# Kernel tuning notes

Measured on AMD Instinct MI355X. Metric: run time of the kernel, lower is better.

Reference implementation:

```python
import jax, jax.numpy as jnp
import numpy as np

DIM = 1024
NUM_HEADS = 16
HEAD_DIM = 64
SCALE = 1.0 / np.sqrt(float(HEAD_DIM))


def setup_inputs() -> dict:
    key = jax.random.key(0)
    ks = jax.random.split(key, 11)
    B, S, D = 2, 4096, DIM
    glorot = lambda k, shape: jax.random.uniform(
        k, shape, jnp.float32,
        -jnp.sqrt(6.0 / (shape[0] + shape[1])), jnp.sqrt(6.0 / (shape[0] + shape[1])))
    return {
        "x": jax.random.normal(ks[0], (B, S, D), jnp.float32),
        "Wq": glorot(ks[1], (D, NUM_HEADS * HEAD_DIM)),
        "bq": jnp.zeros((NUM_HEADS * HEAD_DIM,), jnp.float32),
        "Wk": glorot(ks[2], (D, NUM_HEADS * HEAD_DIM)),
        "bk": jnp.zeros((NUM_HEADS * HEAD_DIM,), jnp.float32),
        "Wv": glorot(ks[3], (D, NUM_HEADS * HEAD_DIM)),
        "bv": jnp.zeros((NUM_HEADS * HEAD_DIM,), jnp.float32),
        "Wqt": glorot(ks[4], (D, D)),
        "bqt": jnp.zeros((D,), jnp.float32),
        "Wo": glorot(ks[5], (D, D)),
        "bo": jnp.zeros((D,), jnp.float32),
        "num_anchor_tokens": 512,
    }


def _split_heads(t):
    # [B, T, H*Dh] -> [B, H, T, Dh]
    B, T, _ = t.shape
    return t.reshape(B, T, NUM_HEADS, HEAD_DIM).transpose(0, 2, 1, 3)


def reference(x, Wq, bq, Wk, bk, Wv, bv, Wqt, bqt, Wo, bo, num_anchor_tokens):
    B, S, D = x.shape
    A = num_anchor_tokens  # static Python int
    anchors = x[:, :A, :]            # [B, A, D]
    queries = x[:, A:, :]            # [B, S-A, D]

    anchor_q = _split_heads(anchors @ Wq + bq)   # [B, H, A, Dh]
    anchor_k = _split_heads(anchors @ Wk + bk)   # [B, H, A, Dh]
    anchor_v = _split_heads(anchors @ Wv + bv)   # [B, H, A, Dh]
    query_q = _split_heads(queries @ Wqt + bqt)  # [B, H, S-A, Dh]

    combined_q = jnp.concatenate([anchor_q, query_q], axis=2)  # [B, H, S, Dh]
    scores = jnp.einsum("bhsd,bhad->bhsa", combined_q, anchor_k) * SCALE
    attn = jax.nn.softmax(scores, axis=-1)        # [B, H, S, A]
    out = jnp.einsum("bhsa,bhad->bhsd", attn, anchor_v)  # [B, H, S, Dh]
    out = out.transpose(0, 2, 1, 3).reshape(B, S, D)
    return out @ Wo + bo
```

## Files before the change

kernel.cpp:

```cpp
#include <hip/hip_runtime.h>
#include <hip/hip_bf16.h>
#include <math.h>
#include <stdint.h>

typedef _Float16 f16;
typedef _Float16 f16x8 __attribute__((ext_vector_type(8)));
typedef _Float16 f16x4 __attribute__((ext_vector_type(4)));
typedef float f32x4 __attribute__((ext_vector_type(4)));

#define DIM   1024
#define NH    16
#define HD    64
#define BB    2
#define SS    4096
#define AA    512
#define SCALE 0.125f
#define EXP_C1 0.18033688011112043f
#define EXP_C2 (-2.8853900817779268f)

#define GLOAD_LDS16(g, l)                                                                   \
  __builtin_amdgcn_global_load_lds((const __attribute__((address_space(1))) uint32_t*)(g),  \
                                   (__attribute__((address_space(3))) uint32_t*)(l), 16, 0, 0)

static const size_t OFF_XH  = 0;
static const size_t OFF_WT  = 8388608;
static const size_t OFF_QC  = OFF_WT + 5u*1048576u;
static const size_t OFF_KB  = OFF_QC + 8388608u;
static const size_t OFF_VT  = OFF_KB + 1048576u;
static const size_t OFF_AO  = OFF_VT + 1048576u;

__global__ __launch_bounds__(256) void cast_x_kernel(const float* __restrict__ x,
                                                     f16* __restrict__ xh) {
    size_t i = ((size_t)blockIdx.x * 256 + threadIdx.x) * 4;
    float4 v = *reinterpret_cast<const float4*>(x + i);
    f16x4 o;
    o[0] = (f16)v.x; o[1] = (f16)v.y; o[2] = (f16)v.z; o[3] = (f16)v.w;
    *reinterpret_cast<f16x4*>(xh + i) = o;
}

__global__ __launch_bounds__(256) void wcast_kernel(const float* W0, const float* W1,
                                                    const float* W2, const float* W3,
                                                    const float* W4,
                                                    f16* T0, f16* T1, f16* T2, f16* T3, f16* T4) {
    __shared__ float tile[32][33];
    const float* W; f16* T;
    switch (blockIdx.z) {
        case 0: W = W0; T = T0; break;
        case 1: W = W1; T = T1; break;
        case 2: W = W2; T = T2; break;
        case 3: W = W3; T = T3; break;
        default: W = W4; T = T4; break;
    }
    int tx = threadIdx.x, ty = threadIdx.y;
    int gx = blockIdx.x * 32, gy = blockIdx.y * 32;
#pragma unroll
    for (int i = 0; i < 32; i += 8)
        tile[ty + i][tx] = W[(size_t)(gy + ty + i) * DIM + gx + tx];
    __syncthreads();
#pragma unroll
    for (int i = 0; i < 32; i += 8)
        T[(size_t)(gx + ty + i) * DIM + gy + tx] = (f16)tile[tx][ty + i];
}

#define G_STAGE(buf, k0)                                               \
    {                                                                  \
        GLOAD_LDS16(Ap + (k0), &As[buf][wid << 9]);                    \
        GLOAD_LDS16(Ap + (k0) + (size_t)64 * DIM,                      \
                    &As[buf][(wid << 9) + 2048]);                      \
        GLOAD_LDS16(Bp + (k0), &Bs[buf][wid << 9]);                    \
        GLOAD_LDS16(Bp + (k0) + (size_t)64 * DIM,                      \
                    &Bs[buf][(wid << 9) + 2048]);                      \
    }

#define G_KLOOP                                                                                   \
    G_STAGE(0, 0);                                                                                \
    __syncthreads();                                                                              \
    int cur = 0;                                                                                  \
    for (int k0 = 0; k0 < DIM; k0 += 32) {                                                        \
        if (k0 + 32 < DIM) G_STAGE(cur ^ 1, k0 + 32);                                             \
        f16x8 af[4], bf[4];                                                                       \
        _Pragma("unroll")                                                                         \
        for (int m = 0; m < 4; m++) {                                                             \
            const int r = wr + m * 16 + lr;                                                       \
            af[m] = *reinterpret_cast<const f16x8*>(&As[cur][r * 32 + ((lg ^ ((r >> 1) & 3)) << 3)]); \
        }                                                                                         \
        _Pragma("unroll")                                                                         \
        for (int n = 0; n < 4; n++) {                                                             \
            const int r = wc + n * 16 + lr;                                                       \
            bf[n] = *reinterpret_cast<const f16x8*>(&Bs[cur][r * 32 + ((lg ^ ((r >> 1) & 3)) << 3)]); \
        }                                                                                         \
        _Pragma("unroll")                                                                         \
        for (int m = 0; m < 4; m++)                                                               \
            _Pragma("unroll")                                                                     \
            for (int n = 0; n < 4; n++)                                                           \
                acc[m][n] = __builtin_amdgcn_mfma_f32_16x16x32_f16(af[m], bf[n], acc[m][n], 0, 0, 0); \
        __syncthreads();                                                                          \
        cur ^= 1;                                                                                 \
    }

__global__ __launch_bounds__(256) void proj_kernel(const f16* __restrict__ xh,
                                                   const f16* __restrict__ wtq,
                                                   const f16* __restrict__ wtqt,
                                                   const f16* __restrict__ wtk,
                                                   const f16* __restrict__ wtv,
                                                   const float* __restrict__ bq,
                                                   const float* __restrict__ bqt,
                                                   const float* __restrict__ bk,
                                                   const float* __restrict__ bv,
                                                   f16* __restrict__ qc,
                                                   f16* __restrict__ kbuf,
                                                   f16* __restrict__ vtb) {
    __shared__ __align__(16) f16 As[2][4096];
    __shared__ __align__(16) f16 Bs[2][4096];

    const int t    = threadIdx.x;
    const int wid  = t >> 6;
    const int lane = t & 63;
    const int lr   = lane & 15;
    const int lg   = lane >> 4;
    const int x    = blockIdx.x, bc = blockIdx.y;

    int b, srow0, mode, sdim;
    const f16* Bt; const float* bias; f16* outp;
    if (x < 64) {
        b = x >> 5; srow0 = (x & 31) * 128;
        if (srow0 < 512) { Bt = wtq; bias = bq; } else { Bt = wtqt; bias = bqt; }
        mode = 0; sdim = SS; outp = qc;
    } else if (x < 72) {
        int y = x - 64; b = y >> 2; srow0 = (y & 3) * 128;
        Bt = wtk; bias = bk; mode = 0; sdim = AA; outp = kbuf;
    } else {
        int y = x - 72; b = y >> 2; srow0 = (y & 3) * 128;
        Bt = wtv; bias = bv; mode = 1; sdim = AA; outp = vtb;
    }

    const int srow = (wid << 4) + (lane >> 2);
    const int sch  = ((lane & 3) ^ ((lane >> 3) & 3)) << 3;
    const f16* Ap = xh + ((size_t)b * SS + srow0 + srow) * DIM + sch;
    const f16* Bp = Bt + ((size_t)(bc * 128 + srow)) * DIM + sch;

    const int wr = (wid >> 1) * 64;
    const int wc = (wid & 1) * 64;

    f32x4 acc[4][4] = {};
    G_KLOOP

#pragma unroll
    for (int m = 0; m < 4; m++) {
        const int row_local = wr + m * 16 + lg * 4;
#pragma unroll
        for (int n = 0; n < 4; n++) {
            const int c  = bc * 128 + wc + n * 16 + lr;
            const float bvv = bias[c];
            const int h = c >> 6, d = c & 63;
#pragma unroll
            for (int q = 0; q < 4; q++) {
                const int s_g = srow0 + row_local + q;
                const float val = acc[m][n][q] + bvv;
                if (mode == 0)
                    outp[(((size_t)(b * NH + h)) * sdim + s_g) * HD + d] = (f16)val;
                else
                    outp[(((size_t)(b * NH + h)) * HD + d) * AA + s_g] = (f16)val;
            }
        }
    }
}

__global__ __launch_bounds__(256) void final_gemm(const f16* __restrict__ ao,
                                                  const f16* __restrict__ wto,
                                                  const float* __restrict__ bo,
                                                  float* __restrict__ out) {
    __shared__ __align__(16) f16 As[2][4096];
    __shared__ __align__(16) f16 Bs[2][4096];

    const int t    = threadIdx.x;
    const int wid  = t >> 6;
    const int lane = t & 63;
    const int lr   = lane & 15;
    const int lg   = lane >> 4;
    const int br   = blockIdx.x, bc = blockIdx.y;

    const int b     = br >> 5;
    const int srow0 = (br & 31) * 128;

    const int srow = (wid << 4) + (lane >> 2);
    const int sch  = ((lane & 3) ^ ((lane >> 3) & 3)) << 3;
    const f16* Ap = ao + ((size_t)b * SS + srow0 + srow) * DIM + sch;
    const f16* Bp = wto + ((size_t)(bc * 128 + srow)) * DIM + sch;

    const int wr = (wid >> 1) * 64;
    const int wc = (wid & 1) * 64;

    f32x4 acc[4][4] = {};
    G_KLOOP

#pragma unroll
    for (int m = 0; m < 4; m++) {
        const int row_local = wr + m * 16 + lg * 4;
#pragma unroll
        for (int n = 0; n < 4; n++) {
            const int c  = bc * 128 + wc + n * 16 + lr;
            const float bvv = bo[c];
#pragma unroll
            for (int q = 0; q < 4; q++)
                out[((size_t)b * SS + srow0 + row_local + q) * DIM + c] = acc[m][n][q] + bvv;
        }
    }
}

__global__ __launch_bounds__(256) void attn_kernel(const f16* __restrict__ qc,
                                                   const f16* __restrict__ kb,
                                                   const f16* __restrict__ vt,
                                                   f16* __restrict__ ao) {
    __shared__ __align__(16) f16 Ks[2][64 * 64];
    __shared__ __align__(16) f16 Vs[2][64 * 64];
    __shared__ __align__(16) f16 Ps[4][16][64];

    const int t    = threadIdx.x;
    const int wid  = t >> 6;
    const int lane = t & 63;
    const int lr   = lane & 15;
    const int lg   = lane >> 4;
    const int qt   = blockIdx.x;
    const int h    = blockIdx.y;
    const int b    = blockIdx.z;
    const size_t bh = (size_t)b * NH + h;

    f16x8 qa[2][2];
#pragma unroll
    for (int g = 0; g < 2; g++) {
        const int qrow = qt * 128 + wid * 32 + g * 16 + lr;
        const f16* qp = qc + (bh * SS + qrow) * HD + lg * 8;
        qa[g][0] = *reinterpret_cast<const f16x8*>(qp);
        qa[g][1] = *reinterpret_cast<const f16x8*>(qp + 32);
    }

    const int sr_k = wid * 16 + (lane >> 3);
    const f16* kg = kb + bh * (size_t)AA * HD;
    const f16* vg = vt + bh * (size_t)HD * AA;

    f32x4 acc[2][4] = {};
    float rsum[2][4] = {};

#define ATTN_STAGE(buf, a0)                                                          \
    {                                                                                \
        _Pragma("unroll")                                                            \
        for (int i = 0; i < 2; i++) {                                                \
            const int r  = sr_k + i * 8;                                             \
            const int ck = (((lane & 7) ^ (r & 7)) << 3);                            \
            GLOAD_LDS16(kg + (size_t)((a0) + r) * HD + ck,                           \
                        &Ks[buf][(wid * 16 + i * 8) * 64]);                          \
            GLOAD_LDS16(vg + (size_t)r * AA + (a0) + ck,                             \
                        &Vs[buf][(wid * 16 + i * 8) * 64]);                          \
        }                                                                            \
    }

    ATTN_STAGE(0, 0);
    __syncthreads();

    int cur = 0;
    for (int at = 0; at < AA / 64; ++at) {
        if (at < AA / 64 - 1) ATTN_STAGE(cur ^ 1, (at + 1) * 64);

        f32x4 s[2][4];
#pragma unroll
        for (int n = 0; n < 4; n++) {
            const int r = n * 16 + lr;
            const int xk = r & 7;
            f16x8 kf0 = *reinterpret_cast<const f16x8*>(&Ks[cur][r * 64 + ((lg ^ xk) << 3)]);
            f16x8 kf1 = *reinterpret_cast<const f16x8*>(&Ks[cur][r * 64 + (((lg + 4) ^ xk) << 3)]);
#pragma unroll
            for (int g = 0; g < 2; g++) {
                f32x4 z = {};
                z = __builtin_amdgcn_mfma_f32_16x16x32_f16(qa[g][0], kf0, z, 0, 0, 0);
                z = __builtin_amdgcn_mfma_f32_16x16x32_f16(qa[g][1], kf1, z, 0, 0, 0);
                s[g][n] = z;
            }
        }

#pragma unroll
        for (int g = 0; g < 2; g++) {
#pragma unroll
            for (int n = 0; n < 4; n++) {
#pragma unroll
                for (int q = 0; q < 4; q++) {
                    const float p = exp2f(fmaf(s[g][n][q], EXP_C1, EXP_C2));
                    rsum[g][q] += p;
                    const int row = lg * 4 + q;
                    Ps[wid][row][(((2 * n + (lr >> 3)) ^ (row & 7)) << 3) + (lr & 7)] = (f16)p;
                }
            }
            const f16x8 pa0 = *reinterpret_cast<const f16x8*>(&Ps[wid][lr][(lg ^ (lr & 7)) << 3]);
            const f16x8 pa1 = *reinterpret_cast<const f16x8*>(&Ps[wid][lr][((lg + 4) ^ (lr & 7)) << 3]);
#pragma unroll
            for (int n = 0; n < 4; n++) {
                const int d = n * 16 + lr;
                const int xv = d & 7;
                f16x8 vf0 = *reinterpret_cast<const f16x8*>(&Vs[cur][d * 64 + ((lg ^ xv) << 3)]);
                f16x8 vf1 = *reinterpret_cast<const f16x8*>(&Vs[cur][d * 64 + (((lg + 4) ^ xv) << 3)]);
                acc[g][n] = __builtin_amdgcn_mfma_f32_16x16x32_f16(pa0, vf0, acc[g][n], 0, 0, 0);
                acc[g][n] = __builtin_amdgcn_mfma_f32_16x16x32_f16(pa1, vf1, acc[g][n], 0, 0, 0);
            }
        }

        __syncthreads();
        cur ^= 1;
    }

#pragma unroll
    for (int off = 1; off < 16; off <<= 1)
#pragma unroll
        for (int g = 0; g < 2; g++)
#pragma unroll
            for (int q = 0; q < 4; q++) rsum[g][q] += __shfl_xor(rsum[g][q], off);

#pragma unroll
    for (int g = 0; g < 2; g++)
#pragma unroll
        for (int q = 0; q < 4; q++) {
            const float inv = 1.0f / rsum[g][q];
            const int row = qt * 128 + wid * 32 + g * 16 + lg * 4 + q;
#pragma unroll
            for (int n = 0; n < 4; n++)
                ao[((size_t)b * SS + row) * DIM + h * HD + n * 16 + lr] = (f16)(acc[g][n][q] * inv);
        }
}

extern "C" void kernel_launch(void* const* d_in, const int* in_sizes, int n_in,
                              void* d_out, int out_size, void* d_ws, size_t ws_size,
                              hipStream_t stream) {
    const float* x   = (const float*)d_in[0];
    const float* Wq  = (const float*)d_in[1];
    const float* bq  = (const float*)d_in[2];
    const float* Wk  = (const float*)d_in[3];
    const float* bk  = (const float*)d_in[4];
    const float* Wv  = (const float*)d_in[5];
    const float* bv  = (const float*)d_in[6];
    const float* Wqt = (const float*)d_in[7];
    const float* bqt = (const float*)d_in[8];
    const float* Wo  = (const float*)d_in[9];
    const float* bo  = (const float*)d_in[10];

    f16* ws   = (f16*)d_ws;
    f16* xh   = ws + OFF_XH;
    f16* wtq  = ws + OFF_WT;
    f16* wtk  = wtq + 1048576u;
    f16* wtv  = wtk + 1048576u;
    f16* wtqt = wtv + 1048576u;
    f16* wto  = wtqt + 1048576u;
    f16* qc   = ws + OFF_QC;
    f16* kbuf = ws + OFF_KB;
    f16* vtb  = ws + OFF_VT;
    f16* ao   = ws + OFF_AO;

    cast_x_kernel<<<8192, 256, 0, stream>>>(x, xh);
    wcast_kernel<<<dim3(32, 32, 5), dim3(32, 8), 0, stream>>>(Wq, Wk, Wv, Wqt, Wo,
                                                              wtq, wtk, wtv, wtqt, wto);

    proj_kernel<<<dim3(80, 8), 256, 0, stream>>>(xh, wtq, wtqt, wtk, wtv,
                                                 bq, bqt, bk, bv, qc, kbuf, vtb);

    attn_kernel<<<dim3(32, NH, BB), 256, 0, stream>>>(qc, kbuf, vtb, ao);

    final_gemm<<<dim3(64, 8), 256, 0, stream>>>(ao, wto, bo, (float*)d_out);
}
```

Baseline: 127.5 us.

## Transpose attention MFMA operands, halve queries per block, pack P stores

Swaps the operand order in the attention MFMAs so each lane holds scores for one query row. This lets the P tile be written with packed 4-wide f16 stores via cvt_pkrtz, and the row-sum needs only two shuffles instead of a 16-lane reduction. Each wave now handles 16 query rows instead of 32 and the grid doubles to 64 blocks in x. That gives more blocks and lower register pressure, at the cost of reloading the K/V tiles from global memory twice as often. The output is also written as packed f16x4 stores.

```diff
diff --git a/kernel.cpp b/kernel.cpp
--- a/kernel.cpp
+++ b/kernel.cpp
@@ -6,6 +6,7 @@
 typedef _Float16 f16;
 typedef _Float16 f16x8 __attribute__((ext_vector_type(8)));
 typedef _Float16 f16x4 __attribute__((ext_vector_type(4)));
+typedef _Float16 f16x2 __attribute__((ext_vector_type(2)));
 typedef float f32x4 __attribute__((ext_vector_type(4)));
 
 #define DIM   1024
@@ -17,6 +18,10 @@
 #define SCALE 0.125f
 #define EXP_C1 0.18033688011112043f
 #define EXP_C2 (-2.8853900817779268f)
+
+static __device__ __forceinline__ f16x2 pkrtz(float a, float b) {
+    return __builtin_bit_cast(f16x2, __builtin_amdgcn_cvt_pkrtz(a, b));
+}
 
 #define GLOAD_LDS16(g, l)                                                                   \
   __builtin_amdgcn_global_load_lds((const __attribute__((address_space(1))) uint32_t*)(g),  \
@@ -214,7 +219,7 @@
                                                    f16* __restrict__ ao) {
     __shared__ __align__(16) f16 Ks[2][64 * 64];
     __shared__ __align__(16) f16 Vs[2][64 * 64];
-    __shared__ __align__(16) f16 Ps[4][16][64];
+    __shared__ __align__(16) f16 Ps[4][16 * 64];
 
     const int t    = threadIdx.x;
     const int wid  = t >> 6;
@@ -226,21 +231,17 @@
     const int b    = blockIdx.z;
     const size_t bh = (size_t)b * NH + h;
 
-    f16x8 qa[2][2];
-#pragma unroll
-    for (int g = 0; g < 2; g++) {
-        const int qrow = qt * 128 + wid * 32 + g * 16 + lr;
-        const f16* qp = qc + (bh * SS + qrow) * HD + lg * 8;
-        qa[g][0] = *reinterpret_cast<const f16x8*>(qp);
-        qa[g][1] = *reinterpret_cast<const f16x8*>(qp + 32);
-    }
+    const int qrow = qt * 64 + wid * 16 + lr;
+    const f16* qp = qc + (bh * SS + qrow) * HD + lg * 8;
+    const f16x8 qa0 = *reinterpret_cast<const f16x8*>(qp);
+    const f16x8 qa1 = *reinterpret_cast<const f16x8*>(qp + 32);
 
     const int sr_k = wid * 16 + (lane >> 3);
     const f16* kg = kb + bh * (size_t)AA * HD;
     const f16* vg = vt + bh * (size_t)HD * AA;
 
-    f32x4 acc[2][4] = {};
-    float rsum[2][4] = {};
+    f32x4 accT[4] = {};
+    float rsum = 0.f;
 
 #define ATTN_STAGE(buf, a0)                                                          \
     {                                                                                \
@@ -258,72 +259,67 @@
     ATTN_STAGE(0, 0);
     __syncthreads();
 
+    f16* PsW = &Ps[wid][0];
+    const int psx = 2 * (lr & 3);
+
     int cur = 0;
     for (int at = 0; at < AA / 64; ++at) {
         if (at < AA / 64 - 1) ATTN_STAGE(cur ^ 1, (at + 1) * 64);
 
-        f32x4 s[2][4];
+        f32x4 s[4];
 #pragma unroll
         for (int n = 0; n < 4; n++) {
             const int r = n * 16 + lr;
             const int xk = r & 7;
             f16x8 kf0 = *reinterpret_cast<const f16x8*>(&Ks[cur][r * 64 + ((lg ^ xk) << 3)]);
             f16x8 kf1 = *reinterpret_cast<const f16x8*>(&Ks[cur][r * 64 + (((lg + 4) ^ xk) << 3)]);
-#pragma unroll
-            for (int g = 0; g < 2; g++) {
-                f32x4 z = {};
-                z = __builtin_amdgcn_mfma_f32_16x16x32_f16(qa[g][0], kf0, z, 0, 0, 0);
-                z = __builtin_amdgcn_mfma_f32_16x16x32_f16(qa[g][1], kf1, z, 0, 0, 0);
-                s[g][n] = z;
-            }
-        }
-
-#pragma unroll
-        for (int g = 0; g < 2; g++) {
-#pragma unroll
-            for (int n = 0; n < 4; n++) {
-#pragma unroll
-                for (int q = 0; q < 4; q++) {
-                    const float p = exp2f(fmaf(s[g][n][q], EXP_C1, EXP_C2));
-                    rsum[g][q] += p;
-                    const int row = lg * 4 + q;
-                    Ps[wid][row][(((2 * n + (lr >> 3)) ^ (row & 7)) << 3) + (lr & 7)] = (f16)p;
-                }
-            }
-            const f16x8 pa0 = *reinterpret_cast<const f16x8*>(&Ps[wid][lr][(lg ^ (lr & 7)) << 3]);
-            const f16x8 pa1 = *reinterpret_cast<const f16x8*>(&Ps[wid][lr][((lg + 4) ^ (lr & 7)) << 3]);
-#pragma unroll
-            for (int n = 0; n < 4; n++) {
-                const int d = n * 16 + lr;
-                const int xv = d & 7;
-                f16x8 vf0 = *reinterpret_cast<const f16x8*>(&Vs[cur][d * 64 + ((lg ^ xv) << 3)]);
-                f16x8 vf1 = *reinterpret_cast<const f16x8*>(&Vs[cur][d * 64 + (((lg + 4) ^ xv) << 3)]);
-                acc[g][n] = __builtin_amdgcn_mfma_f32_16x16x32_f16(pa0, vf0, acc[g][n], 0, 0, 0);
-                acc[g][n] = __builtin_amdgcn_mfma_f32_16x16x32_f16(pa1, vf1, acc[g][n], 0, 0, 0);
-            }
+            f32x4 z = {};
+            z = __builtin_amdgcn_mfma_f32_16x16x32_f16(kf0, qa0, z, 0, 0, 0);
+            z = __builtin_amdgcn_mfma_f32_16x16x32_f16(kf1, qa1, z, 0, 0, 0);
+            s[n] = z;
+        }
+
+#pragma unroll
+        for (int n = 0; n < 4; n++) {
+            const float p0 = exp2f(fmaf(s[n][0], EXP_C1, EXP_C2));
+            const float p1 = exp2f(fmaf(s[n][1], EXP_C1, EXP_C2));
+            const float p2 = exp2f(fmaf(s[n][2], EXP_C1, EXP_C2));
+            const float p3 = exp2f(fmaf(s[n][3], EXP_C1, EXP_C2));
+            rsum += (p0 + p1) + (p2 + p3);
+            const f16x2 w0 = pkrtz(p0, p1);
+            const f16x2 w1 = pkrtz(p2, p3);
+            f16x4 w; w[0] = w0[0]; w[1] = w0[1]; w[2] = w1[0]; w[3] = w1[1];
+            *reinterpret_cast<f16x4*>(&PsW[lr * 64 + (((4 * n + lg) ^ psx) << 2)]) = w;
+        }
+        const f16x8 pa0 = *reinterpret_cast<const f16x8*>(&PsW[lr * 64 + (((2 * lg) ^ psx) << 2)]);
+        const f16x8 pa1 = *reinterpret_cast<const f16x8*>(&PsW[lr * 64 + (((8 + 2 * lg) ^ psx) << 2)]);
+
+#pragma unroll
+        for (int nd = 0; nd < 4; nd++) {
+            const int d = nd * 16 + lr;
+            const int xv = d & 7;
+            f16x8 vf0 = *reinterpret_cast<const f16x8*>(&Vs[cur][d * 64 + ((lg ^ xv) << 3)]);
+            f16x8 vf1 = *reinterpret_cast<const f16x8*>(&Vs[cur][d * 64 + (((lg + 4) ^ xv) << 3)]);
+            accT[nd] = __builtin_amdgcn_mfma_f32_16x16x32_f16(vf0, pa0, accT[nd], 0, 0, 0);
+            accT[nd] = __builtin_amdgcn_mfma_f32_16x16x32_f16(vf1, pa1, accT[nd], 0, 0, 0);
         }
 
         __syncthreads();
         cur ^= 1;
     }
 
-#pragma unroll
-    for (int off = 1; off < 16; off <<= 1)
-#pragma unroll
-        for (int g = 0; g < 2; g++)
-#pragma unroll
-            for (int q = 0; q < 4; q++) rsum[g][q] += __shfl_xor(rsum[g][q], off);
-
-#pragma unroll
-    for (int g = 0; g < 2; g++)
-#pragma unroll
-        for (int q = 0; q < 4; q++) {
-            const float inv = 1.0f / rsum[g][q];
-            const int row = qt * 128 + wid * 32 + g * 16 + lg * 4 + q;
-#pragma unroll
-            for (int n = 0; n < 4; n++)
-                ao[((size_t)b * SS + row) * DIM + h * HD + n * 16 + lr] = (f16)(acc[g][n][q] * inv);
-        }
+    rsum += __shfl_xor(rsum, 16);
+    rsum += __shfl_xor(rsum, 32);
+    const float inv = 1.0f / rsum;
+
+    f16* aop = ao + ((size_t)b * SS + qrow) * DIM + h * HD + lg * 4;
+#pragma unroll
+    for (int nd = 0; nd < 4; nd++) {
+        const f16x2 w0 = pkrtz(accT[nd][0] * inv, accT[nd][1] * inv);
+        const f16x2 w1 = pkrtz(accT[nd][2] * inv, accT[nd][3] * inv);
+        f16x4 w; w[0] = w0[0]; w[1] = w0[1]; w[2] = w1[0]; w[3] = w1[1];
+        *reinterpret_cast<f16x4*>(aop + nd * 16) = w;
+    }
 }
 
 extern "C" void kernel_launch(void* const* d_in, const int* in_sizes, int n_in,
@@ -360,7 +356,7 @@
     proj_kernel<<<dim3(80, 8), 256, 0, stream>>>(xh, wtq, wtqt, wtk, wtv,
                                                  bq, bqt, bk, bv, qc, kbuf, vtb);
 
-    attn_kernel<<<dim3(32, NH, BB), 256, 0, stream>>>(qc, kbuf, vtb, ao);
+    attn_kernel<<<dim3(64, NH, BB), 256, 0, stream>>>(qc, kbuf, vtb, ao);
 
     final_gemm<<<dim3(64, 8), 256, 0, stream>>>(ao, wto, bo, (float*)d_out);
 }
```

Measured after the change: 119.1 us. 1.07x faster.
